# Performance work log

Hardware: AMD Instinct MI355X
Metric: run time of the kernel (lower is better)

Reference implementation:

```python
import jax, jax.numpy as jnp
import numpy as np

N, DM, F, G, FG = 4096, 512, 128, 8, 16
DH, DE, ES = 128, 256, 4
E = G * ES
GROUP_TOP_K, EXPERT_TOP_K = 2, 2
TEMP = 1.0
LN_EPS = 1e-5


def _ln(x, g, b):
    m = jnp.mean(x, axis=-1, keepdims=True)
    v = jnp.mean((x - m) ** 2, axis=-1, keepdims=True)
    return (x - m) * jax.lax.rsqrt(v + LN_EPS) * g + b


def _topk_softmax(logits, k):
    # faithful to torch _topk_softmax: softmax over top-k values, zeros elsewhere
    vals, idx = jax.lax.top_k(logits, k)
    w = jax.nn.softmax(vals, axis=-1)
    oh = jax.nn.one_hot(idx, logits.shape[-1], dtype=logits.dtype)  # [..., k, E]
    return jnp.einsum('...ke,...k->...e', oh, w)


def setup_inputs() -> dict:
    key = jax.random.key(0)
    ks = iter(jax.random.split(key, 32))
    n = lambda shape, s=0.02: jax.random.normal(next(ks), shape, dtype=jnp.float32) * s
    d = {
        'hidden': jax.random.normal(next(ks), (N, DM), dtype=jnp.float32),
        'feat': jax.random.normal(next(ks), (N, F), dtype=jnp.float32),
        # pre_ln
        'pre_ln_g': jnp.ones((DM,), jnp.float32), 'pre_ln_b': jnp.zeros((DM,), jnp.float32),
        # router_hidden_encoder: LN(DM) -> Lin(DM,DH) -> GELU -> Lin(DH,DH)
        'rh_ln_g': jnp.ones((DM,), jnp.float32), 'rh_ln_b': jnp.zeros((DM,), jnp.float32),
        'rh_w1': n((DM, DH)), 'rh_b1': jnp.zeros((DH,), jnp.float32),
        'rh_w2': n((DH, DH)), 'rh_b2': jnp.zeros((DH,), jnp.float32),
        # stage_feature_encoder: LN(F) -> Lin(F,DH) -> GELU -> Lin(DH,DH)
        'sf_ln_g': jnp.ones((F,), jnp.float32), 'sf_ln_b': jnp.zeros((F,), jnp.float32),
        'sf_w1': n((F, DH)), 'sf_b1': jnp.zeros((DH,), jnp.float32),
        'sf_w2': n((DH, DH)), 'sf_b2': jnp.zeros((DH,), jnp.float32),
        # group_feature_encoders (stacked over G): LN(FG) -> Lin(FG,DH) -> GELU -> Lin(DH,DH)
        'gf_ln_g': jnp.ones((G, FG), jnp.float32), 'gf_ln_b': jnp.zeros((G, FG), jnp.float32),
        'gf_w1': n((G, FG, DH)), 'gf_b1': jnp.zeros((G, DH), jnp.float32),
        'gf_w2': n((G, DH, DH)), 'gf_b2': jnp.zeros((G, DH), jnp.float32),
        # per_group_scorer (ScalarRouter): Lin(4DH,DH) -> GELU -> Lin(DH,1)
        'pgs_w1': n((4 * DH, DH)), 'pgs_b1': jnp.zeros((DH,), jnp.float32),
        'pgs_w2': n((DH,)), 'pgs_b2': jnp.zeros((), jnp.float32),
        # intra_routers (stacked over G): Lin(4DH,DH) -> GELU -> Lin(DH,ES)
        'ir_w1': n((G, 4 * DH, DH)), 'ir_b1': jnp.zeros((G, DH), jnp.float32),
        'ir_w2': n((G, DH, ES)), 'ir_b2': jnp.zeros((G, ES), jnp.float32),
        # experts (stacked over E = G*ES, group-major): Lin(DM,DE) -> GELU -> Lin(DE,DM)
        'ex_w1': n((E, DM, DE)), 'ex_b1': jnp.zeros((E, DE), jnp.float32),
        'ex_w2': n((E, DE, DM)), 'ex_b2': jnp.zeros((E, DM), jnp.float32),
    }
    return d


def reference(hidden, feat, pre_ln_g, pre_ln_b, rh_ln_g, rh_ln_b, rh_w1, rh_b1, rh_w2, rh_b2,
              sf_ln_g, sf_ln_b, sf_w1, sf_b1, sf_w2, sf_b2,
              gf_ln_g, gf_ln_b, gf_w1, gf_b1, gf_w2, gf_b2,
              pgs_w1, pgs_b1, pgs_w2, pgs_b2,
              ir_w1, ir_b1, ir_w2, ir_b2,
              ex_w1, ex_b1, ex_w2, ex_b2):
    # expert input (pre-LN hidden)
    h_norm = _ln(hidden, pre_ln_g, pre_ln_b)                         # [N, DM]

    # factorized router encoders
    h_enc = jax.nn.gelu(_ln(hidden, rh_ln_g, rh_ln_b) @ rh_w1 + rh_b1) @ rh_w2 + rh_b2   # [N, DH]
    s_enc = jax.nn.gelu(_ln(feat, sf_ln_g, sf_ln_b) @ sf_w1 + sf_b1) @ sf_w2 + sf_b2     # [N, DH]
    gfeat = feat.reshape(N, G, FG)                                    # disjoint contiguous group features
    g_h = jax.nn.gelu(jnp.einsum('ngf,gfh->ngh', _ln(gfeat, gf_ln_g, gf_ln_b), gf_w1) + gf_b1)
    g_enc = jnp.einsum('ngh,ghk->ngk', g_h, gf_w2) + gf_b2            # [N, G, DH]

    hB = jnp.broadcast_to(h_enc[:, None, :], (N, G, DH))
    sB = jnp.broadcast_to(s_enc[:, None, :], (N, G, DH))
    router_in = jnp.concatenate([hB, sB, g_enc, hB * g_enc], axis=-1)  # [N, G, 4DH]

    # per-group scalar scores -> group logits -> top-k scatter softmax
    pg_h = jax.nn.gelu(jnp.einsum('ngi,ih->ngh', router_in, pgs_w1) + pgs_b1)
    group_logits = (jnp.einsum('ngh,h->ng', pg_h, pgs_w2) + pgs_b2) / max(TEMP, 1e-6)    # [N, G]
    group_w = _topk_softmax(group_logits, GROUP_TOP_K)                 # [N, G]

    # intra-group expert routers -> top-k scatter softmax over expert_scale
    ir_h = jax.nn.gelu(jnp.einsum('ngi,gih->ngh', router_in, ir_w1) + ir_b1)
    intra_logits = jnp.einsum('ngh,ghe->nge', ir_h, ir_w2) + ir_b2     # [N, G, ES]
    intra_w = _topk_softmax(intra_logits, EXPERT_TOP_K)                # [N, G, ES]

    comb_w = (group_w[:, :, None] * intra_w).reshape(N, E)             # group-major expert order

    # per-expert GELU MLPs on pre-LN hidden (dense compute, sparse weights)
    eh = jax.nn.gelu(jnp.einsum('nd,edh->neh', h_norm, ex_w1) + ex_b1) # [N, E, DE]
    eo = jnp.einsum('neh,ehd->ned', eh, ex_w2) + ex_b2                 # [N, E, DM]
    out = jnp.einsum('ne,ned->nd', comb_w, eo)                         # [N, DM]
    return out
```

## Files before the change

### kernel.cpp

```cpp
#include <hip/hip_runtime.h>
#include <hip/hip_bf16.h>
#include <math.h>

#define N_TOK 4096
#define DM 512
#define FDIM 128
#define G 8
#define FG 16
#define DH 128
#define DE 256
#define ES 4
#define E_EXP 32
#define LN_EPS 1e-5f
#define BT 32

typedef __attribute__((ext_vector_type(8))) short bf16x8;
typedef __attribute__((ext_vector_type(4))) float f32x4;

#define MFMA16(a, b, c) __builtin_amdgcn_mfma_f32_16x16x32_bf16((a), (b), (c), 0, 0, 0)

#define PSTRIDE 6144

__device__ __forceinline__ float gelu_t(float x) {
    const float c = 0.7978845608028654f;
    float x3 = x * x * x;
    return 0.5f * x * (1.0f + tanhf(c * (x + 0.044715f * x3)));
}

__device__ __forceinline__ short f2bf(float f) {
    __hip_bfloat16 h = __float2bfloat16(f);
    return *reinterpret_cast<short*>(&h);
}
__device__ __forceinline__ float bf2f(short s) {
    __hip_bfloat16 h = *reinterpret_cast<__hip_bfloat16*>(&s);
    return __bfloat162float(h);
}
__device__ __forceinline__ void split3(float x, short& h, short& m, short& l) {
    h = f2bf(x);
    float r = x - bf2f(h);
    m = f2bf(r);
    float r2 = r - bf2f(m);
    l = f2bf(r2);
}

__device__ __forceinline__ void gload_lds16(const void* g, void* l) {
    __builtin_amdgcn_global_load_lds(
        (const __attribute__((address_space(1))) unsigned int*)g,
        (__attribute__((address_space(3))) unsigned int*)l, 16, 0, 0);
}

struct ConvJob { const float* src; short* dh; short* dm; short* dl;
                 int KB, NB, Kreal, plain, blk0; };
struct ConvJobs { ConvJob j[10]; };

__global__ void k_pre(ConvJobs J, int nconv,
                      const float* __restrict__ hidden,
                      const float* __restrict__ pg, const float* __restrict__ pb,
                      const float* __restrict__ rg, const float* __restrict__ rb,
                      __hip_bfloat16* __restrict__ h_normb, float* __restrict__ hL) {
    int b = blockIdx.x;
    if (b >= nconv) {
        int n = b - nconv;
        int j = threadIdx.x;
        const float* x = hidden + (size_t)n * DM;
        float v0 = x[j], v1 = x[j + 256];
        float s = v0 + v1, q = v0 * v0 + v1 * v1;
#pragma unroll
        for (int o = 32; o; o >>= 1) { s += __shfl_down(s, o); q += __shfl_down(q, o); }
        __shared__ float red[8];
        int w = j >> 6;
        if ((j & 63) == 0) { red[w] = s; red[4 + w] = q; }
        __syncthreads();
        float sum = red[0] + red[1] + red[2] + red[3];
        float sq  = red[4] + red[5] + red[6] + red[7];
        float m = sum * (1.0f / DM);
        float var = sq * (1.0f / DM) - m * m;
        float rs = rsqrtf(var + LN_EPS);
        float t0 = (v0 - m) * rs, t1 = (v1 - m) * rs;
        size_t base = (size_t)n * DM;
        h_normb[base + j]       = __float2bfloat16(t0 * pg[j]       + pb[j]);
        h_normb[base + j + 256] = __float2bfloat16(t1 * pg[j + 256] + pb[j + 256]);
        hL[base + j]           = t0 * rg[j]       + rb[j];
        hL[base + j + 256]     = t1 * rg[j + 256] + rb[j + 256];
        return;
    }
    int ji = 0;
#pragma unroll
    for (int i = 1; i < 10; i++) if (b >= J.j[i].blk0) ji = i;
    const ConvJob jb = J.j[ji];
    int rel = b - jb.blk0;
    int mat = rel / jb.KB, kb = rel % jb.KB;
    int ncols = jb.NB * 16;
    const float* s = jb.src + (size_t)mat * jb.Kreal * ncols;
    size_t dbase = ((size_t)mat * jb.KB + kb) * jb.NB * 512;
    for (int p = threadIdx.x; p < jb.NB * 64; p += 256) {
        int nb = p >> 6, lane = p & 63;
        int row0 = kb * 32 + ((lane >> 4) << 3);
        int col = nb * 16 + (lane & 15);
        if (jb.plain) {
            union { short sh[8]; uint4 v; } t;
#pragma unroll
            for (int j = 0; j < 8; j++) {
                float x = (row0 + j < jb.Kreal) ? s[(size_t)(row0 + j) * ncols + col] : 0.f;
                t.sh[j] = f2bf(x);
            }
            *(uint4*)&jb.dh[dbase + (size_t)p * 8] = t.v;
        } else {
            union { short sh[8]; uint4 v; } hi, mi, lo;
#pragma unroll
            for (int j = 0; j < 8; j++) {
                float x = (row0 + j < jb.Kreal) ? s[(size_t)(row0 + j) * ncols + col] : 0.f;
                split3(x, hi.sh[j], mi.sh[j], lo.sh[j]);
            }
            *(uint4*)&jb.dh[dbase + (size_t)p * 8] = hi.v;
            *(uint4*)&jb.dm[dbase + (size_t)p * 8] = mi.v;
            *(uint4*)&jb.dl[dbase + (size_t)p * 8] = lo.v;
        }
    }
}

__device__ __forceinline__ void emit_split_tiles(
        int tid, short (*Ah)[136], short (*Am)[136], short (*Al)[136],
        short* __restrict__ Yt, size_t panel0 ) {
    int lane_ = tid & 63, w = tid >> 6;
#pragma unroll
    for (int j = 0; j < 6; j++) {
        int combo = w * 6 + j;
        int split = combo >> 3;
        int rem = combo & 7; int t16 = rem >> 2, kb = rem & 3;
        const short* sp = (split == 0) ? &Ah[0][0] : (split == 1) ? &Am[0][0] : &Al[0][0];
        uint4 v = *(const uint4*)&sp[(t16 * 16 + (lane_ & 15)) * 136 + kb * 32 + (lane_ >> 4) * 8];
        *(uint4*)&Yt[((panel0 + t16) * 4 + kb) * 1536 + split * 512 + lane_ * 8] = v;
    }
}

template <int KB_TOT, bool DO_LN>
__device__ __forceinline__ void enc2_body(
        int bx, char* smem,
        const float* __restrict__ X,
        const float* __restrict__ lng, const float* __restrict__ lnb,
        const short* __restrict__ W1h, const short* __restrict__ W1m, const short* __restrict__ W1l,
        const float* __restrict__ B1,
        const short* __restrict__ W2h, const short* __restrict__ W2m, const short* __restrict__ W2l,
        const float* __restrict__ B2,
        short* __restrict__ Yt) {
    constexpr int K = KB_TOT * 32;
    const int n0 = bx * 32;
    const int tid = threadIdx.x;
    const int wave = tid >> 6, lane = tid & 63;
    const int quad = lane >> 4, lm = lane & 15;
    const int mt = wave & 1;
    const int ngb = (wave >> 1) * 4;

    short (*Ah)[136] = (short(*)[136])smem;
    short (*Am)[136] = (short(*)[136])(smem + 8704);
    short (*Al)[136] = (short(*)[136])(smem + 2 * 8704);

    f32x4 acc[4];
#pragma unroll
    for (int i = 0; i < 4; i++) acc[i] = (f32x4)(0.f);

    if (DO_LN) {
        for (int idx = tid; idx < 1024; idx += 256) {
            int row = idx >> 5, c4 = (idx & 31) * 4;
            float4 v = *(const float4*)&X[(size_t)(n0 + row) * K + c4];
            float s = v.x + v.y + v.z + v.w;
            float q = v.x * v.x + v.y * v.y + v.z * v.z + v.w * v.w;
#pragma unroll
            for (int o = 16; o; o >>= 1) { s += __shfl_xor(s, o); q += __shfl_xor(q, o); }
            float mean = s * (1.0f / 128.0f);
            float var = q * (1.0f / 128.0f) - mean * mean;
            float rs = rsqrtf(var + LN_EPS);
            float xv[4] = {(v.x - mean) * rs * lng[c4 + 0] + lnb[c4 + 0],
                           (v.y - mean) * rs * lng[c4 + 1] + lnb[c4 + 1],
                           (v.z - mean) * rs * lng[c4 + 2] + lnb[c4 + 2],
                           (v.w - mean) * rs * lng[c4 + 3] + lnb[c4 + 3]};
#pragma unroll
            for (int j = 0; j < 4; j++) {
                short h, m, l; split3(xv[j], h, m, l);
                Ah[row][c4 + j] = h; Am[row][c4 + j] = m; Al[row][c4 + j] = l;
            }
        }
        __syncthreads();
#pragma unroll
        for (int kb = 0; kb < KB_TOT; kb++) {
            bf16x8 ah = *(const bf16x8*)&Ah[mt * 16 + lm][kb * 32 + quad * 8];
            bf16x8 am = *(const bf16x8*)&Am[mt * 16 + lm][kb * 32 + quad * 8];
            bf16x8 al = *(const bf16x8*)&Al[mt * 16 + lm][kb * 32 + quad * 8];
#pragma unroll
            for (int nt = 0; nt < 4; nt++) {
                size_t bi = (((size_t)kb * 8 + ngb + nt) * 64 + lane) * 8;
                bf16x8 bh = *(const bf16x8*)&W1h[bi];
                bf16x8 bm = *(const bf16x8*)&W1m[bi];
                bf16x8 bl = *(const bf16x8*)&W1l[bi];
                acc[nt] = MFMA16(al, bh, acc[nt]);
                acc[nt] = MFMA16(am, bm, acc[nt]);
                acc[nt] = MFMA16(ah, bl, acc[nt]);
                acc[nt] = MFMA16(am, bh, acc[nt]);
                acc[nt] = MFMA16(ah, bm, acc[nt]);
                acc[nt] = MFMA16(ah, bh, acc[nt]);
            }
        }
    } else {
        for (int kb = 0; kb < KB_TOT; kb++) {
            const float* xs = X + (size_t)(n0 + mt * 16 + lm) * K + kb * 32 + quad * 8;
            float4 x0 = *(const float4*)xs, x1 = *(const float4*)(xs + 4);
            float xv[8] = {x0.x, x0.y, x0.z, x0.w, x1.x, x1.y, x1.z, x1.w};
            bf16x8 ah, am, al;
#pragma unroll
            for (int j = 0; j < 8; j++) {
                short h, m, l; split3(xv[j], h, m, l);
                ah[j] = h; am[j] = m; al[j] = l;
            }
#pragma unroll
            for (int nt = 0; nt < 4; nt++) {
                size_t bi = (((size_t)kb * 8 + ngb + nt) * 64 + lane) * 8;
                bf16x8 bh = *(const bf16x8*)&W1h[bi];
                bf16x8 bm = *(const bf16x8*)&W1m[bi];
                bf16x8 bl = *(const bf16x8*)&W1l[bi];
                acc[nt] = MFMA16(al, bh, acc[nt]);
                acc[nt] = MFMA16(am, bm, acc[nt]);
                acc[nt] = MFMA16(ah, bl, acc[nt]);
                acc[nt] = MFMA16(am, bh, acc[nt]);
                acc[nt] = MFMA16(ah, bm, acc[nt]);
                acc[nt] = MFMA16(ah, bh, acc[nt]);
            }
        }
    }
    __syncthreads();
#pragma unroll
    for (int nt = 0; nt < 4; nt++) {
        int col = (ngb + nt) * 16 + lm;
        float b1 = B1[col];
#pragma unroll
        for (int r = 0; r < 4; r++) {
            int row = mt * 16 + quad * 4 + r;
            short h, m, l; split3(gelu_t(acc[nt][r] + b1), h, m, l);
            Ah[row][col] = h; Am[row][col] = m; Al[row][col] = l;
        }
    }
    __syncthreads();
    f32x4 acc2[4];
#pragma unroll
    for (int i = 0; i < 4; i++) acc2[i] = (f32x4)(0.f);
#pragma unroll
    for (int kb = 0; kb < 4; kb++) {
        bf16x8 ah = *(const bf16x8*)&Ah[mt * 16 + lm][kb * 32 + quad * 8];
        bf16x8 am = *(const bf16x8*)&Am[mt * 16 + lm][kb * 32 + quad * 8];
        bf16x8 al = *(const bf16x8*)&Al[mt * 16 + lm][kb * 32 + quad * 8];
#pragma unroll
        for (int nt = 0; nt < 4; nt++) {
            size_t bi = (((size_t)kb * 8 + ngb + nt) * 64 + lane) * 8;
            bf16x8 bh = *(const bf16x8*)&W2h[bi];
            bf16x8 bm = *(const bf16x8*)&W2m[bi];
            bf16x8 bl = *(const bf16x8*)&W2l[bi];
            acc2[nt] = MFMA16(al, bh, acc2[nt]);
            acc2[nt] = MFMA16(am, bm, acc2[nt]);
            acc2[nt] = MFMA16(ah, bl, acc2[nt]);
            acc2[nt] = MFMA16(am, bh, acc2[nt]);
            acc2[nt] = MFMA16(ah, bm, acc2[nt]);
            acc2[nt] = MFMA16(ah, bh, acc2[nt]);
        }
    }
    __syncthreads();
#pragma unroll
    for (int nt = 0; nt < 4; nt++) {
        int col = (ngb + nt) * 16 + lm;
        float b2 = B2[col];
#pragma unroll
        for (int r = 0; r < 4; r++) {
            int row = mt * 16 + quad * 4 + r;
            short h, m, l; split3(acc2[nt][r] + b2, h, m, l);
            Ah[row][col] = h; Am[row][col] = m; Al[row][col] = l;
        }
    }
    __syncthreads();
    emit_split_tiles(tid, Ah, Am, Al, Yt, (size_t)bx * 2);
}

__device__ __forceinline__ void genc_one(
        int bx, int g, char* smem,
        const float* __restrict__ feat,
        const float* __restrict__ gln_g, const float* __restrict__ gln_b,
        const short* __restrict__ W1h, const short* __restrict__ W1m, const short* __restrict__ W1l,
        const float* __restrict__ gb1,
        const short* __restrict__ W2h, const short* __restrict__ W2m, const short* __restrict__ W2l,
        const float* __restrict__ gb2,
        short* __restrict__ Gs) {
    const int tid = threadIdx.x;
    const int wave = tid >> 6, lane = tid & 63;
    const int quad = lane >> 4, lm = lane & 15;
    const int mt = wave & 1;
    const int ngb = (wave >> 1) * 4;
    const int n0 = bx * 32;

    short (*Ah)[136] = (short(*)[136])smem;
    short (*Am)[136] = (short(*)[136])(smem + 8704);
    short (*Al)[136] = (short(*)[136])(smem + 2 * 8704);

    {
        int t = tid >> 3, sub = tid & 7;
        const float* fr = feat + (size_t)(n0 + t) * FDIM + g * FG;
        float xv[FG];
        float mean = 0.f;
#pragma unroll
        for (int i = 0; i < FG; i++) { xv[i] = fr[i]; mean += xv[i]; }
        mean *= (1.0f / FG);
        float var = 0.f;
#pragma unroll
        for (int i = 0; i < FG; i++) { float d = xv[i] - mean; var += d * d; }
        var *= (1.0f / FG);
        float rs = rsqrtf(var + LN_EPS);
#pragma unroll
        for (int j = 0; j < 2; j++) {
            int i = sub * 2 + j;
            float xn = (xv[i] - mean) * rs * gln_g[g * FG + i] + gln_b[g * FG + i];
            short h, m, l; split3(xn, h, m, l);
            Ah[t][i] = h; Am[t][i] = m; Al[t][i] = l;
            Ah[t][16 + i] = 0; Am[t][16 + i] = 0; Al[t][16 + i] = 0;
        }
    }
    __syncthreads();
    f32x4 acc[4];
#pragma unroll
    for (int i = 0; i < 4; i++) acc[i] = (f32x4)(0.f);
    {
        bf16x8 ah = *(const bf16x8*)&Ah[mt * 16 + lm][quad * 8];
        bf16x8 am = *(const bf16x8*)&Am[mt * 16 + lm][quad * 8];
        bf16x8 al = *(const bf16x8*)&Al[mt * 16 + lm][quad * 8];
#pragma unroll
        for (int nt = 0; nt < 4; nt++) {
            size_t bi = (((size_t)g * 8 + ngb + nt) * 64 + lane) * 8;
            bf16x8 bh = *(const bf16x8*)&W1h[bi];
            bf16x8 bm = *(const bf16x8*)&W1m[bi];
            bf16x8 bl = *(const bf16x8*)&W1l[bi];
            acc[nt] = MFMA16(al, bh, acc[nt]);
            acc[nt] = MFMA16(am, bm, acc[nt]);
            acc[nt] = MFMA16(ah, bl, acc[nt]);
            acc[nt] = MFMA16(am, bh, acc[nt]);
            acc[nt] = MFMA16(ah, bm, acc[nt]);
            acc[nt] = MFMA16(ah, bh, acc[nt]);
        }
    }
    __syncthreads();
#pragma unroll
    for (int nt = 0; nt < 4; nt++) {
        int col = (ngb + nt) * 16 + lm;
        float b1 = gb1[g * DH + col];
#pragma unroll
        for (int r = 0; r < 4; r++) {
            int row = mt * 16 + quad * 4 + r;
            short h, m, l; split3(gelu_t(acc[nt][r] + b1), h, m, l);
            Ah[row][col] = h; Am[row][col] = m; Al[row][col] = l;
        }
    }
    __syncthreads();
    f32x4 acc2[4];
#pragma unroll
    for (int i = 0; i < 4; i++) acc2[i] = (f32x4)(0.f);
#pragma unroll
    for (int kb = 0; kb < 4; kb++) {
        bf16x8 a2h = *(const bf16x8*)&Ah[mt * 16 + lm][kb * 32 + quad * 8];
        bf16x8 a2m = *(const bf16x8*)&Am[mt * 16 + lm][kb * 32 + quad * 8];
        bf16x8 a2l = *(const bf16x8*)&Al[mt * 16 + lm][kb * 32 + quad * 8];
#pragma unroll
        for (int nt = 0; nt < 4; nt++) {
            size_t bi = ((((size_t)g * 4 + kb) * 8 + ngb + nt) * 64 + lane) * 8;
            bf16x8 bh = *(const bf16x8*)&W2h[bi];
            bf16x8 bm = *(const bf16x8*)&W2m[bi];
            bf16x8 bl = *(const bf16x8*)&W2l[bi];
            acc2[nt] = MFMA16(a2l, bh, acc2[nt]);
            acc2[nt] = MFMA16(a2m, bm, acc2[nt]);
            acc2[nt] = MFMA16(a2h, bl, acc2[nt]);
            acc2[nt] = MFMA16(a2m, bh, acc2[nt]);
            acc2[nt] = MFMA16(a2h, bm, acc2[nt]);
            acc2[nt] = MFMA16(a2h, bh, acc2[nt]);
        }
    }
    __syncthreads();
#pragma unroll
    for (int nt = 0; nt < 4; nt++) {
        int col = (ngb + nt) * 16 + lm;
        float b2 = gb2[g * DH + col];
#pragma unroll
        for (int r = 0; r < 4; r++) {
            int row = mt * 16 + quad * 4 + r;
            short h, m, l; split3(acc2[nt][r] + b2, h, m, l);
            Ah[row][col] = h; Am[row][col] = m; Al[row][col] = l;
        }
    }
    __syncthreads();
    emit_split_tiles(tid, Ah, Am, Al, Gs, (size_t)g * 256 + bx * 2);
}

__global__ __launch_bounds__(256) void k_enc_all(
        const float* __restrict__ hL, const float* __restrict__ feat,
        const float* __restrict__ sf_g, const float* __restrict__ sf_b,
        const float* __restrict__ gln_g, const float* __restrict__ gln_b,
        const short* Brh1H, const short* Brh1M, const short* Brh1L, const float* rh_b1,
        const short* Brh2H, const short* Brh2M, const short* Brh2L, const float* rh_b2,
        const short* Bsf1H, const short* Bsf1M, const short* Bsf1L, const float* sf_b1,
        const short* Bsf2H, const short* Bsf2M, const short* Bsf2L, const float* sf_b2,
        const short* Bgf1H, const short* Bgf1M, const short* Bgf1L, const float* gf_b1,
        const short* Bgf2H, const short* Bgf2M, const short* Bgf2L, const float* gf_b2,
        short* __restrict__ Hs, short* __restrict__ Ss, short* __restrict__ Gs) {
    __shared__ __align__(16) char smem[3 * 8704];
    int bid = blockIdx.x;
    if (bid < 128)
        enc2_body<16, false>(bid, smem, hL, nullptr, nullptr,
                             Brh1H, Brh1M, Brh1L, rh_b1, Brh2H, Brh2M, Brh2L, rh_b2, Hs);
    else if (bid < 256)
        enc2_body<4, true>(bid - 128, smem, feat, sf_g, sf_b,
                           Bsf1H, Bsf1M, Bsf1L, sf_b1, Bsf2H, Bsf2M, Bsf2L, sf_b2, Ss);
    else {
        int idx = bid - 256;
        genc_one(idx >> 3, idx & 7, smem, feat, gln_g, gln_b,
                 Bgf1H, Bgf1M, Bgf1L, gf_b1, Bgf2H, Bgf2M, Bgf2L, gf_b2, Gs);
    }
}

__global__ __launch_bounds__(512) void k_router_mfma(
        const short* __restrict__ Hs, const short* __restrict__ Ss, const short* __restrict__ Gs,
        const short* __restrict__ BpgH, const short* __restrict__ BpgM, const short* __restrict__ BpgL,
        const short* __restrict__ BirH, const short* __restrict__ BirM, const short* __restrict__ BirL,
        const float* __restrict__ pb1, const float* __restrict__ pw2, const float* __restrict__ pb2,
        const float* __restrict__ ib1, const float* __restrict__ iw2, const float* __restrict__ ib2,
        float* __restrict__ glog, float* __restrict__ ilog) {
    const int g = blockIdx.x & 7;
    const int bx = blockIdx.x >> 3;
    const int n0 = bx * 64;
    const int tid = threadIdx.x;
    const int wave = tid >> 6, lane = tid & 63;
    const int quad = lane >> 4, lm = lane & 15;
    const bool is_pg = wave < 4;
    const int nbase = (wave & 3) * 2;
    const short* Bh = is_pg ? BpgH : (BirH + (size_t)g * 65536);
    const short* Bm = is_pg ? BpgM : (BirM + (size_t)g * 65536);
    const short* Bl = is_pg ? BpgL : (BirL + (size_t)g * 65536);

    const short* HsB = Hs + (size_t)bx * 4 * PSTRIDE;
    const short* SsB = Ss + (size_t)bx * 4 * PSTRIDE;
    const short* GsB = Gs + ((size_t)g * 256 + bx * 4) * PSTRIDE;

    __shared__ __align__(16) char smem[49152];

    f32x4 acc[4][2];
#pragma unroll
    for (int mt = 0; mt < 4; mt++)
#pragma unroll
        for (int nt = 0; nt < 2; nt++) acc[mt][nt] = (f32x4)(0.f);

    for (int ch = 0; ch < 4; ch++) {
        __syncthreads();
        if (ch < 3) {
            const short* base = (ch == 0) ? HsB : (ch == 1) ? SsB : GsB;
#pragma unroll
            for (int it = 0; it < 6; it++) {
                int combo = wave * 6 + it;
                int split = combo >> 4;
                int rem = combo & 15; int kbl = rem >> 2, t16 = rem & 3;
                const short* gp = base + (size_t)t16 * PSTRIDE + kbl * 1536 + split * 512 + lane * 8;
                char* lp = smem + split * 16384 + kbl * 4096 + t16 * 1024;
                gload_lds16(gp, lp);
            }
        } else {
            for (int idx = tid; idx < 1024; idx += 512) {
                int kbl = idx >> 8, rem = idx & 255;
                int t16 = rem >> 6, lane2 = rem & 63;
                size_t loff = (size_t)kbl * 4096 + t16 * 1024 + (size_t)lane2 * 16;
                bf16x8 gh = *(const bf16x8*)(smem + loff);
                bf16x8 gm = *(const bf16x8*)(smem + 16384 + loff);
                bf16x8 gl = *(const bf16x8*)(smem + 32768 + loff);
                const short* hp = HsB + (size_t)t16 * PSTRIDE + kbl * 1536 + lane2 * 8;
                bf16x8 hh8 = *(const bf16x8*)hp;
                bf16x8 hm8 = *(const bf16x8*)(hp + 512);
                bf16x8 hl8 = *(const bf16x8*)(hp + 1024);
                union { short sh[8]; uint4 v; } oh, om, ol;
#pragma unroll
                for (int j = 0; j < 8; j++) {
                    float gv = bf2f(gh[j]) + bf2f(gm[j]) + bf2f(gl[j]);
                    float hv = bf2f(hh8[j]) + bf2f(hm8[j]) + bf2f(hl8[j]);
                    short a_, b_, c_; split3(hv * gv, a_, b_, c_);
                    oh.sh[j] = a_; om.sh[j] = b_; ol.sh[j] = c_;
                }
                *(uint4*)(smem + loff) = oh.v;
                *(uint4*)(smem + 16384 + loff) = om.v;
                *(uint4*)(smem + 32768 + loff) = ol.v;
            }
        }
        __syncthreads();
#pragma unroll
        for (int kbl = 0; kbl < 4; kbl++) {
            int kb = ch * 4 + kbl;
            bf16x8 Ahf[4], Amf[4], Alf[4];
#pragma unroll
            for (int mt = 0; mt < 4; mt++) {
                size_t loff = (size_t)kbl * 4096 + mt * 1024 + (size_t)lane * 16;
                Ahf[mt] = *(const bf16x8*)(smem + loff);
                Amf[mt] = *(const bf16x8*)(smem + 16384 + loff);
                Alf[mt] = *(const bf16x8*)(smem + 32768 + loff);
            }
#pragma unroll
            for (int nt = 0; nt < 2; nt++) {
                int nb = nbase + nt;
                size_t bi = (((size_t)kb * 8 + nb) * 64 + lane) * 8;
                bf16x8 bh = *(const bf16x8*)&Bh[bi];
                bf16x8 bm = *(const bf16x8*)&Bm[bi];
                bf16x8 bl = *(const bf16x8*)&Bl[bi];
#pragma unroll
                for (int mt = 0; mt < 4; mt++) {
                    acc[mt][nt] = MFMA16(Alf[mt], bh, acc[mt][nt]);
                    acc[mt][nt] = MFMA16(Amf[mt], bm, acc[mt][nt]);
                    acc[mt][nt] = MFMA16(Ahf[mt], bl, acc[mt][nt]);
                    acc[mt][nt] = MFMA16(Amf[mt], bh, acc[mt][nt]);
                    acc[mt][nt] = MFMA16(Ahf[mt], bm, acc[mt][nt]);
                    acc[mt][nt] = MFMA16(Ahf[mt], bh, acc[mt][nt]);
                }
            }
        }
    }

    float (*ph)[129] = (float(*)[129])smem;
    float (*ih)[129] = (float(*)[129])(smem + 32 * 129 * 4);
    for (int h = 0; h < 2; h++) {
        __syncthreads();
#pragma unroll
        for (int mi = 0; mi < 2; mi++) {
            int mt = 2 * h + mi;
#pragma unroll
            for (int nt = 0; nt < 2; nt++) {
                int col = (nbase + nt) * 16 + lm;
                float b1 = is_pg ? pb1[col] : ib1[g * DH + col];
                float* dst = is_pg ? &ph[0][0] : &ih[0][0];
#pragma unroll
                for (int r = 0; r < 4; r++) {
                    int row = mi * 16 + quad * 4 + r;
                    dst[row * 129 + col] = gelu_t(acc[mt][nt][r] + b1);
                }
            }
        }
        __syncthreads();
        if (tid < 128) {
            int t = tid >> 2, q = tid & 3;
            float s = 0.f;
            for (int i = q * 32; i < q * 32 + 32; i++) s += ph[t][i] * pw2[i];
            s += __shfl_xor(s, 1);
            s += __shfl_xor(s, 2);
            if (q == 0) glog[(size_t)(n0 + h * 32 + t) * G + g] = s + pb2[0];
        } else if (tid < 384) {
            int t2 = tid - 128;
            int t = t2 >> 3, e = (t2 >> 1) & 3, half = t2 & 1;
            const float* wv = iw2 + (size_t)g * DH * ES;
            float s = 0.f;
            for (int i = half * 64; i < half * 64 + 64; i++) s += ih[t][i] * wv[i * ES + e];
            s += __shfl_xor(s, 1);
            if (half == 0) ilog[((size_t)(n0 + h * 32 + t) * G + g) * ES + e] = s + ib2[g * ES + e];
        }
    }
}

__global__ void k_topk(const float* __restrict__ glog, const float* __restrict__ ilog,
                       int* __restrict__ cnt, int* __restrict__ toks, float* __restrict__ wgts) {
    int n = blockIdx.x * blockDim.x + threadIdx.x;
    if (n >= N_TOK) return;
    float gl[G];
#pragma unroll
    for (int g = 0; g < G; g++) gl[g] = glog[(size_t)n * G + g];
    int i1 = 0; float v1 = gl[0];
#pragma unroll
    for (int g = 1; g < G; g++) if (gl[g] > v1) { v1 = gl[g]; i1 = g; }
    int i2 = -1; float v2 = -1e30f;
#pragma unroll
    for (int g = 0; g < G; g++) if (g != i1 && gl[g] > v2) { v2 = gl[g]; i2 = g; }
    float eg = expf(v2 - v1);
    float den = 1.0f / (1.0f + eg);
    float gw_sel[2] = { den, eg * den };
    int g_sel[2] = { i1, i2 };
#pragma unroll
    for (int s = 0; s < 2; s++) {
        int g = g_sel[s]; float gw = gw_sel[s];
        float il[ES];
#pragma unroll
        for (int e = 0; e < ES; e++) il[e] = ilog[((size_t)n * G + g) * ES + e];
        int j1 = 0; float u1 = il[0];
#pragma unroll
        for (int e = 1; e < ES; e++) if (il[e] > u1) { u1 = il[e]; j1 = e; }
        int j2 = -1; float u2 = -1e30f;
#pragma unroll
        for (int e = 0; e < ES; e++) if (e != j1 && il[e] > u2) { u2 = il[e]; j2 = e; }
        float ei = expf(u2 - u1);
        float d2 = 1.0f / (1.0f + ei);
        int ex1 = g * ES + j1, ex2 = g * ES + j2;
        int p1 = atomicAdd(&cnt[ex1], 1);
        toks[(size_t)ex1 * N_TOK + p1] = n * 4 + s * 2;     wgts[(size_t)ex1 * N_TOK + p1] = gw * d2;
        int p2 = atomicAdd(&cnt[ex2], 1);
        toks[(size_t)ex2 * N_TOK + p2] = n * 4 + s * 2 + 1; wgts[(size_t)ex2 * N_TOK + p2] = gw * ei * d2;
    }
}

__global__ __launch_bounds__(512) void k_expert_mfma(
        const __hip_bfloat16* __restrict__ h_normb,
        const short* __restrict__ wB1, const float* __restrict__ eb1,
        const short* __restrict__ wB2, const float* __restrict__ eb2,
        const int* __restrict__ cnt, const int* __restrict__ toks,
        const float* __restrict__ wgts, float* __restrict__ part) {
    const int e = blockIdx.x & 31;
    const int slot = blockIdx.x >> 5;
    const int c = cnt[e];
    const int start = slot * BT;
    if (start >= c) return;
    const int m = min(BT, c - start);

    __shared__ short hs[BT][520];
    short (*es)[264] = (short(*)[264])&hs[0][0];
    __shared__ int   tok_s[BT];
    __shared__ float w_s[BT];

    const int tid = threadIdx.x;
    if (tid < BT) {
        bool ok = tid < m;
        tok_s[tid] = ok ? toks[(size_t)e * N_TOK + start + tid] : 0;
        w_s[tid]   = ok ? wgts[(size_t)e * N_TOK + start + tid] : 0.f;
    }
    __syncthreads();
    for (int idx = tid; idx < BT * 64; idx += 512) {
        int t = idx >> 6, ch = idx & 63;
        uint4 v = make_uint4(0, 0, 0, 0);
        if (t < m) v = *((const uint4*)(h_normb + (size_t)(tok_s[t] >> 2) * DM) + ch);
        *(uint4*)&hs[t][ch * 8] = v;
    }
    __syncthreads();

    const int wave = tid >> 6, lane = tid & 63;
    const int quad = lane >> 4, lm = lane & 15;

    const int ng = wave * 2;
    f32x4 acc1[2][2];
#pragma unroll
    for (int a = 0; a < 2; a++)
#pragma unroll
        for (int b = 0; b < 2; b++) acc1[a][b] = (f32x4)(0.f);
    {
        const short* w1e = wB1 + (size_t)e * DM * DE;
        for (int kb = 0; kb < 16; kb++) {
            bf16x8 a0 = *(const bf16x8*)&hs[lm][kb * 32 + quad * 8];
            bf16x8 a1 = *(const bf16x8*)&hs[16 + lm][kb * 32 + quad * 8];
            const short* wp = w1e + ((size_t)kb * 16 + ng) * 512 + lane * 8;
#pragma unroll
            for (int nt = 0; nt < 2; nt++) {
                bf16x8 b = *(const bf16x8*)(wp + nt * 512);
                acc1[0][nt] = MFMA16(a0, b, acc1[0][nt]);
                acc1[1][nt] = MFMA16(a1, b, acc1[1][nt]);
            }
        }
    }
    __syncthreads();
#pragma unroll
    for (int nt = 0; nt < 2; nt++) {
        int col = (ng + nt) * 16 + lm;
        float b1 = eb1[e * DE + col];
#pragma unroll
        for (int mt = 0; mt < 2; mt++)
#pragma unroll
        for (int r = 0; r < 4; r++) {
            int row = mt * 16 + quad * 4 + r;
            es[row][col] = f2bf(gelu_t(acc1[mt][nt][r] + b1));
        }
    }
    __syncthreads();

    {
        const int ng2 = wave * 4;
        f32x4 acc[2][4];
#pragma unroll
        for (int a = 0; a < 2; a++)
#pragma unroll
            for (int b = 0; b < 4; b++) acc[a][b] = (f32x4)(0.f);
        const short* w2e = wB2 + (size_t)e * DE * DM;
        for (int kb = 0; kb < 8; kb++) {
            bf16x8 a0 = *(const bf16x8*)&es[lm][kb * 32 + quad * 8];
            bf16x8 a1 = *(const bf16x8*)&es[16 + lm][kb * 32 + quad * 8];
            const short* wp = w2e + ((size_t)kb * 32 + ng2) * 512 + lane * 8;
#pragma unroll
            for (int nt = 0; nt < 4; nt++) {
                bf16x8 b = *(const bf16x8*)(wp + nt * 512);
                acc[0][nt] = MFMA16(a0, b, acc[0][nt]);
                acc[1][nt] = MFMA16(a1, b, acc[1][nt]);
            }
        }
        const float* b2 = eb2 + (size_t)e * DM;
#pragma unroll
        for (int mt = 0; mt < 2; mt++)
#pragma unroll
        for (int r = 0; r < 4; r++) {
            int row = mt * 16 + quad * 4 + r;
            if (row < m) {
                float w = w_s[row];
                float* prow = part + (size_t)tok_s[row] * DM;
#pragma unroll
                for (int nt = 0; nt < 4; nt++) {
                    int col = (ng2 + nt) * 16 + lm;
                    prow[col] = w * (acc[mt][nt][r] + b2[col]);
                }
            }
        }
    }
}

__global__ void k_reduce(const float* __restrict__ part, float* __restrict__ out) {
    int n = blockIdx.x;
    int j = threadIdx.x;
    const float4* p = (const float4*)(part + (size_t)n * 4 * DM);
    float4 a = p[j], b = p[128 + j], c = p[256 + j], d = p[384 + j];
    float4 r = make_float4(a.x + b.x + c.x + d.x, a.y + b.y + c.y + d.y,
                           a.z + b.z + c.z + d.z, a.w + b.w + c.w + d.w);
    ((float4*)(out + (size_t)n * DM))[j] = r;
}

extern "C" void kernel_launch(void* const* d_in, const int* in_sizes, int n_in,
                              void* d_out, int out_size, void* d_ws, size_t ws_size,
                              hipStream_t stream) {
    const float* hidden  = (const float*)d_in[0];
    const float* feat    = (const float*)d_in[1];
    const float* pre_g   = (const float*)d_in[2];
    const float* pre_b   = (const float*)d_in[3];
    const float* rh_g    = (const float*)d_in[4];
    const float* rh_b    = (const float*)d_in[5];
    const float* rh_w1   = (const float*)d_in[6];
    const float* rh_b1   = (const float*)d_in[7];
    const float* rh_w2   = (const float*)d_in[8];
    const float* rh_b2   = (const float*)d_in[9];
    const float* sf_g    = (const float*)d_in[10];
    const float* sf_b    = (const float*)d_in[11];
    const float* sf_w1   = (const float*)d_in[12];
    const float* sf_b1   = (const float*)d_in[13];
    const float* sf_w2   = (const float*)d_in[14];
    const float* sf_b2   = (const float*)d_in[15];
    const float* gln_g   = (const float*)d_in[16];
    const float* gln_b   = (const float*)d_in[17];
    const float* gf_w1   = (const float*)d_in[18];
    const float* gf_b1   = (const float*)d_in[19];
    const float* gf_w2   = (const float*)d_in[20];
    const float* gf_b2   = (const float*)d_in[21];
    const float* pgs_w1  = (const float*)d_in[22];
    const float* pgs_b1  = (const float*)d_in[23];
    const float* pgs_w2  = (const float*)d_in[24];
    const float* pgs_b2  = (const float*)d_in[25];
    const float* ir_w1   = (const float*)d_in[26];
    const float* ir_b1   = (const float*)d_in[27];
    const float* ir_w2   = (const float*)d_in[28];
    const float* ir_b2   = (const float*)d_in[29];
    const float* ex_w1   = (const float*)d_in[30];
    const float* ex_b1   = (const float*)d_in[31];
    const float* ex_w2   = (const float*)d_in[32];
    const float* ex_b2   = (const float*)d_in[33];
    float* out = (float*)d_out;

    char* w = (char*)d_ws;
    auto alloc = [&](size_t bytes) { void* r = (void*)w; w += (bytes + 255) & ~(size_t)255; return r; };
    __hip_bfloat16* h_normb = (__hip_bfloat16*)alloc((size_t)N_TOK * DM * 2);
    short* Hs    = (short*)alloc((size_t)256 * PSTRIDE * 2);
    short* Ss    = (short*)alloc((size_t)256 * PSTRIDE * 2);
    float* glog  = (float*)alloc((size_t)N_TOK * G * 4);
    float* ilog  = (float*)alloc((size_t)N_TOK * G * ES * 4);
    float* wgts  = (float*)alloc((size_t)E_EXP * N_TOK * 4);
    short* wB1   = (short*)alloc((size_t)E_EXP * DM * DE * 2);
    short* wB2   = (short*)alloc((size_t)E_EXP * DE * DM * 2);
    short* BpgH  = (short*)alloc((size_t)16 * 8 * 512 * 2);
    short* BpgM  = (short*)alloc((size_t)16 * 8 * 512 * 2);
    short* BpgL  = (short*)alloc((size_t)16 * 8 * 512 * 2);
    short* BirH  = (short*)alloc((size_t)G * 16 * 8 * 512 * 2);
    short* BirM  = (short*)alloc((size_t)G * 16 * 8 * 512 * 2);
    short* BirL  = (short*)alloc((size_t)G * 16 * 8 * 512 * 2);
    short* Brh1H = (short*)alloc((size_t)16 * 8 * 512 * 2);
    short* Brh1M = (short*)alloc((size_t)16 * 8 * 512 * 2);
    short* Brh1L = (short*)alloc((size_t)16 * 8 * 512 * 2);
    short* Brh2H = (short*)alloc((size_t)4 * 8 * 512 * 2);
    short* Brh2M = (short*)alloc((size_t)4 * 8 * 512 * 2);
    short* Brh2L = (short*)alloc((size_t)4 * 8 * 512 * 2);
    short* Bsf1H = (short*)alloc((size_t)4 * 8 * 512 * 2);
    short* Bsf1M = (short*)alloc((size_t)4 * 8 * 512 * 2);
    short* Bsf1L = (short*)alloc((size_t)4 * 8 * 512 * 2);
    short* Bsf2H = (short*)alloc((size_t)4 * 8 * 512 * 2);
    short* Bsf2M = (short*)alloc((size_t)4 * 8 * 512 * 2);
    short* Bsf2L = (short*)alloc((size_t)4 * 8 * 512 * 2);
    short* Bgf1H = (short*)alloc((size_t)G * 1 * 8 * 512 * 2);
    short* Bgf1M = (short*)alloc((size_t)G * 1 * 8 * 512 * 2);
    short* Bgf1L = (short*)alloc((size_t)G * 1 * 8 * 512 * 2);
    short* Bgf2H = (short*)alloc((size_t)G * 4 * 8 * 512 * 2);
    short* Bgf2M = (short*)alloc((size_t)G * 4 * 8 * 512 * 2);
    short* Bgf2L = (short*)alloc((size_t)G * 4 * 8 * 512 * 2);
    int* cnt     = (int*)alloc(E_EXP * 4);
    int* toks    = (int*)alloc((size_t)E_EXP * N_TOK * 4);
    char* uni   = (char*)alloc((size_t)N_TOK * 4 * DM * 4);
    float* hL   = (float*)uni;
    short* Gs   = (short*)(uni + (size_t)N_TOK * DM * 4);
    float* part = (float*)uni;

    hipMemsetAsync(cnt, 0, E_EXP * sizeof(int), stream);

    ConvJobs J;
    int b0 = 0;
    auto mkjob = [&](int i, const float* s, short* dh, short* dm, short* dl,
                     int KB, int NB, int Kreal, int plain, int nmat) {
        J.j[i] = ConvJob{s, dh, dm, dl, KB, NB, Kreal, plain, b0};
        b0 += KB * nmat;
    };
    mkjob(0, ex_w1, wB1, nullptr, nullptr, 16, 16, 512, 1, E_EXP);
    mkjob(1, ex_w2, wB2, nullptr, nullptr, 8, 32, 256, 1, E_EXP);
    mkjob(2, pgs_w1, BpgH, BpgM, BpgL, 16, 8, 512, 0, 1);
    mkjob(3, ir_w1, BirH, BirM, BirL, 16, 8, 512, 0, G);
    mkjob(4, rh_w1, Brh1H, Brh1M, Brh1L, 16, 8, 512, 0, 1);
    mkjob(5, rh_w2, Brh2H, Brh2M, Brh2L, 4, 8, 128, 0, 1);
    mkjob(6, sf_w1, Bsf1H, Bsf1M, Bsf1L, 4, 8, 128, 0, 1);
    mkjob(7, sf_w2, Bsf2H, Bsf2M, Bsf2L, 4, 8, 128, 0, 1);
    mkjob(8, gf_w1, Bgf1H, Bgf1M, Bgf1L, 1, 8, 16, 0, G);
    mkjob(9, gf_w2, Bgf2H, Bgf2M, Bgf2L, 4, 8, 128, 0, G);
    k_pre<<<b0 + N_TOK, 256, 0, stream>>>(J, b0, hidden, pre_g, pre_b, rh_g, rh_b, h_normb, hL);

    k_enc_all<<<256 + (N_TOK / 32) * G, 256, 0, stream>>>(
        hL, feat, sf_g, sf_b, gln_g, gln_b,
        Brh1H, Brh1M, Brh1L, rh_b1, Brh2H, Brh2M, Brh2L, rh_b2,
        Bsf1H, Bsf1M, Bsf1L, sf_b1, Bsf2H, Bsf2M, Bsf2L, sf_b2,
        Bgf1H, Bgf1M, Bgf1L, gf_b1, Bgf2H, Bgf2M, Bgf2L, gf_b2,
        Hs, Ss, Gs);

    k_router_mfma<<<(N_TOK / 64) * G, 512, 0, stream>>>(Hs, Ss, Gs,
                                             BpgH, BpgM, BpgL, BirH, BirM, BirL,
                                             pgs_b1, pgs_w2, pgs_b2, ir_b1, ir_w2, ir_b2,
                                             glog, ilog);

    k_topk<<<N_TOK / 256, 256, 0, stream>>>(glog, ilog, cnt, toks, wgts);
    k_expert_mfma<<<(N_TOK / BT) * E_EXP, 512, 0, stream>>>(h_normb, wB1, ex_b1, wB2, ex_b2,
                                                            cnt, toks, wgts, part);
    k_reduce<<<N_TOK, 128, 0, stream>>>(part, out);
}
```

Measured before the change: 339.0 us.

## Software-pipeline router operand loads through registers to overlap with MFMA

Replaces the direct global-to-LDS loads in the router kernel with register-staged prefetching. The next chunk's operands are loaded into registers while MFMAs run on the current chunk. The hB*g_enc product chunk is computed from globally loaded H and G values during chunk 2's compute, instead of a separate LDS read-modify-write phase. It also adds a min-blocks-per-CU launch bound, which increases register pressure from the prefetch buffers and risks spills.

```diff
diff --git a/kernel.cpp b/kernel.cpp
--- a/kernel.cpp
+++ b/kernel.cpp
@@ -41,12 +41,6 @@
     m = f2bf(r);
     float r2 = r - bf2f(m);
     l = f2bf(r2);
-}
-
-__device__ __forceinline__ void gload_lds16(const void* g, void* l) {
-    __builtin_amdgcn_global_load_lds(
-        (const __attribute__((address_space(1))) unsigned int*)g,
-        (__attribute__((address_space(3))) unsigned int*)l, 16, 0, 0);
 }
 
 struct ConvJob { const float* src; short* dh; short* dm; short* dl;
@@ -419,7 +413,7 @@
     }
 }
 
-__global__ __launch_bounds__(512) void k_router_mfma(
+__global__ __launch_bounds__(512, 4) void k_router_mfma(
         const short* __restrict__ Hs, const short* __restrict__ Ss, const short* __restrict__ Gs,
         const short* __restrict__ BpgH, const short* __restrict__ BpgM, const short* __restrict__ BpgL,
         const short* __restrict__ BirH, const short* __restrict__ BirM, const short* __restrict__ BirL,
@@ -444,51 +438,62 @@
 
     __shared__ __align__(16) char smem[49152];
 
+    int goff[6];
+#pragma unroll
+    for (int it = 0; it < 6; it++) {
+        int lin = it * 512 + tid;
+        int split = lin >> 10, rem = lin & 1023;
+        int kbl = rem >> 8, t16 = (rem >> 6) & 3, ln = rem & 63;
+        goff[it] = t16 * PSTRIDE + kbl * 1536 + split * 512 + ln * 8;
+    }
+    int roff[2], woff[2];
+#pragma unroll
+    for (int t = 0; t < 2; t++) {
+        int slot = t * 512 + tid;
+        int kbl = slot >> 8, t16 = (slot >> 6) & 3, ln = slot & 63;
+        roff[t] = t16 * PSTRIDE + kbl * 1536 + ln * 8;
+        woff[t] = kbl * 4096 + t16 * 1024 + ln * 16;
+    }
+
     f32x4 acc[4][2];
 #pragma unroll
     for (int mt = 0; mt < 4; mt++)
 #pragma unroll
         for (int nt = 0; nt < 2; nt++) acc[mt][nt] = (f32x4)(0.f);
+
+    bf16x8 R[6];
+    bf16x8 R3[2][3];
+#pragma unroll
+    for (int it = 0; it < 6; it++) R[it] = *(const bf16x8*)(HsB + goff[it]);
 
     for (int ch = 0; ch < 4; ch++) {
         __syncthreads();
         if (ch < 3) {
-            const short* base = (ch == 0) ? HsB : (ch == 1) ? SsB : GsB;
-#pragma unroll
-            for (int it = 0; it < 6; it++) {
-                int combo = wave * 6 + it;
-                int split = combo >> 4;
-                int rem = combo & 15; int kbl = rem >> 2, t16 = rem & 3;
-                const short* gp = base + (size_t)t16 * PSTRIDE + kbl * 1536 + split * 512 + lane * 8;
-                char* lp = smem + split * 16384 + kbl * 4096 + t16 * 1024;
-                gload_lds16(gp, lp);
-            }
+#pragma unroll
+            for (int it = 0; it < 6; it++)
+                *(bf16x8*)(smem + ((it * 512 + tid) * 16)) = R[it];
         } else {
-            for (int idx = tid; idx < 1024; idx += 512) {
-                int kbl = idx >> 8, rem = idx & 255;
-                int t16 = rem >> 6, lane2 = rem & 63;
-                size_t loff = (size_t)kbl * 4096 + t16 * 1024 + (size_t)lane2 * 16;
-                bf16x8 gh = *(const bf16x8*)(smem + loff);
-                bf16x8 gm = *(const bf16x8*)(smem + 16384 + loff);
-                bf16x8 gl = *(const bf16x8*)(smem + 32768 + loff);
-                const short* hp = HsB + (size_t)t16 * PSTRIDE + kbl * 1536 + lane2 * 8;
-                bf16x8 hh8 = *(const bf16x8*)hp;
-                bf16x8 hm8 = *(const bf16x8*)(hp + 512);
-                bf16x8 hl8 = *(const bf16x8*)(hp + 1024);
-                union { short sh[8]; uint4 v; } oh, om, ol;
-#pragma unroll
-                for (int j = 0; j < 8; j++) {
-                    float gv = bf2f(gh[j]) + bf2f(gm[j]) + bf2f(gl[j]);
-                    float hv = bf2f(hh8[j]) + bf2f(hm8[j]) + bf2f(hl8[j]);
-                    short a_, b_, c_; split3(hv * gv, a_, b_, c_);
-                    oh.sh[j] = a_; om.sh[j] = b_; ol.sh[j] = c_;
+#pragma unroll
+            for (int t = 0; t < 2; t++)
+#pragma unroll
+                for (int s = 0; s < 3; s++)
+                    *(bf16x8*)(smem + s * 16384 + woff[t]) = R3[t][s];
+        }
+        __syncthreads();
+        bf16x8 Hv[2][3], Gv[2][3];
+        if (ch < 2) {
+            const short* nb = (ch == 0) ? SsB : GsB;
+#pragma unroll
+            for (int it = 0; it < 6; it++) R[it] = *(const bf16x8*)(nb + goff[it]);
+        } else if (ch == 2) {
+#pragma unroll
+            for (int t = 0; t < 2; t++)
+#pragma unroll
+                for (int s = 0; s < 3; s++) {
+                    Hv[t][s] = *(const bf16x8*)(HsB + roff[t] + s * 512);
+                    Gv[t][s] = *(const bf16x8*)(GsB + roff[t] + s * 512);
                 }
-                *(uint4*)(smem + loff) = oh.v;
-                *(uint4*)(smem + 16384 + loff) = om.v;
-                *(uint4*)(smem + 32768 + loff) = ol.v;
-            }
-        }
-        __syncthreads();
+        }
 #pragma unroll
         for (int kbl = 0; kbl < 4; kbl++) {
             int kb = ch * 4 + kbl;
@@ -516,6 +521,20 @@
                     acc[mt][nt] = MFMA16(Ahf[mt], bm, acc[mt][nt]);
                     acc[mt][nt] = MFMA16(Ahf[mt], bh, acc[mt][nt]);
                 }
+            }
+        }
+        if (ch == 2) {
+#pragma unroll
+            for (int t = 0; t < 2; t++) {
+                bf16x8 oa, ob, oc;
+#pragma unroll
+                for (int j = 0; j < 8; j++) {
+                    float hv = bf2f(Hv[t][0][j]) + bf2f(Hv[t][1][j]) + bf2f(Hv[t][2][j]);
+                    float gv = bf2f(Gv[t][0][j]) + bf2f(Gv[t][1][j]) + bf2f(Gv[t][2][j]);
+                    short a_, b_, c_; split3(hv * gv, a_, b_, c_);
+                    oa[j] = a_; ob[j] = b_; oc[j] = c_;
+                }
+                R3[t][0] = oa; R3[t][1] = ob; R3[t][2] = oc;
             }
         }
     }
```

Measured after the change: 457.7 us. +35.0%, slower.

## Register-prefetch next router-input chunk while computing current chunk

Applied to the files above, without the earlier changes.

Replaces the direct global-to-LDS loads with register-staged prefetch, so each chunk's global loads are issued before the MFMA compute of the previous chunk and then written to LDS. The h*g product chunk is also computed from global loads issued ahead, instead of a separate LDS read-modify-write pass. This is meant to hide global load latency behind MFMA work in the router scoring kernel, at the cost of more VGPRs for the staged registers and possibly lower occupancy.

```diff
diff --git a/kernel.cpp b/kernel.cpp
--- a/kernel.cpp
+++ b/kernel.cpp
@@ -41,12 +41,6 @@
     m = f2bf(r);
     float r2 = r - bf2f(m);
     l = f2bf(r2);
-}
-
-__device__ __forceinline__ void gload_lds16(const void* g, void* l) {
-    __builtin_amdgcn_global_load_lds(
-        (const __attribute__((address_space(1))) unsigned int*)g,
-        (__attribute__((address_space(3))) unsigned int*)l, 16, 0, 0);
 }
 
 struct ConvJob { const float* src; short* dh; short* dm; short* dl;
@@ -444,81 +438,125 @@
 
     __shared__ __align__(16) char smem[49152];
 
+    int goff[6];
+#pragma unroll
+    for (int it = 0; it < 6; it++) {
+        int lin = it * 512 + tid;
+        int split = lin >> 10, rem = lin & 1023;
+        int kbl = rem >> 8, t16 = (rem >> 6) & 3, ln = rem & 63;
+        goff[it] = t16 * PSTRIDE + kbl * 1536 + split * 512 + ln * 8;
+    }
+    int roff0, roff1, woff0, woff1;
+    {
+        int slot = tid;
+        int kbl = slot >> 8, t16 = (slot >> 6) & 3, ln = slot & 63;
+        roff0 = t16 * PSTRIDE + kbl * 1536 + ln * 8;
+        woff0 = kbl * 4096 + t16 * 1024 + ln * 16;
+        slot = 512 + tid;
+        kbl = slot >> 8; t16 = (slot >> 6) & 3; ln = slot & 63;
+        roff1 = t16 * PSTRIDE + kbl * 1536 + ln * 8;
+        woff1 = kbl * 4096 + t16 * 1024 + ln * 16;
+    }
+
     f32x4 acc[4][2];
 #pragma unroll
     for (int mt = 0; mt < 4; mt++)
 #pragma unroll
         for (int nt = 0; nt < 2; nt++) acc[mt][nt] = (f32x4)(0.f);
 
-    for (int ch = 0; ch < 4; ch++) {
-        __syncthreads();
-        if (ch < 3) {
-            const short* base = (ch == 0) ? HsB : (ch == 1) ? SsB : GsB;
-#pragma unroll
-            for (int it = 0; it < 6; it++) {
-                int combo = wave * 6 + it;
-                int split = combo >> 4;
-                int rem = combo & 15; int kbl = rem >> 2, t16 = rem & 3;
-                const short* gp = base + (size_t)t16 * PSTRIDE + kbl * 1536 + split * 512 + lane * 8;
-                char* lp = smem + split * 16384 + kbl * 4096 + t16 * 1024;
-                gload_lds16(gp, lp);
-            }
-        } else {
-            for (int idx = tid; idx < 1024; idx += 512) {
-                int kbl = idx >> 8, rem = idx & 255;
-                int t16 = rem >> 6, lane2 = rem & 63;
-                size_t loff = (size_t)kbl * 4096 + t16 * 1024 + (size_t)lane2 * 16;
-                bf16x8 gh = *(const bf16x8*)(smem + loff);
-                bf16x8 gm = *(const bf16x8*)(smem + 16384 + loff);
-                bf16x8 gl = *(const bf16x8*)(smem + 32768 + loff);
-                const short* hp = HsB + (size_t)t16 * PSTRIDE + kbl * 1536 + lane2 * 8;
-                bf16x8 hh8 = *(const bf16x8*)hp;
-                bf16x8 hm8 = *(const bf16x8*)(hp + 512);
-                bf16x8 hl8 = *(const bf16x8*)(hp + 1024);
-                union { short sh[8]; uint4 v; } oh, om, ol;
-#pragma unroll
-                for (int j = 0; j < 8; j++) {
-                    float gv = bf2f(gh[j]) + bf2f(gm[j]) + bf2f(gl[j]);
-                    float hv = bf2f(hh8[j]) + bf2f(hm8[j]) + bf2f(hl8[j]);
-                    short a_, b_, c_; split3(hv * gv, a_, b_, c_);
-                    oh.sh[j] = a_; om.sh[j] = b_; ol.sh[j] = c_;
-                }
-                *(uint4*)(smem + loff) = oh.v;
-                *(uint4*)(smem + 16384 + loff) = om.v;
-                *(uint4*)(smem + 32768 + loff) = ol.v;
-            }
-        }
-        __syncthreads();
-#pragma unroll
-        for (int kbl = 0; kbl < 4; kbl++) {
-            int kb = ch * 4 + kbl;
-            bf16x8 Ahf[4], Amf[4], Alf[4];
-#pragma unroll
-            for (int mt = 0; mt < 4; mt++) {
-                size_t loff = (size_t)kbl * 4096 + mt * 1024 + (size_t)lane * 16;
-                Ahf[mt] = *(const bf16x8*)(smem + loff);
-                Amf[mt] = *(const bf16x8*)(smem + 16384 + loff);
-                Alf[mt] = *(const bf16x8*)(smem + 32768 + loff);
-            }
-#pragma unroll
-            for (int nt = 0; nt < 2; nt++) {
-                int nb = nbase + nt;
-                size_t bi = (((size_t)kb * 8 + nb) * 64 + lane) * 8;
-                bf16x8 bh = *(const bf16x8*)&Bh[bi];
-                bf16x8 bm = *(const bf16x8*)&Bm[bi];
-                bf16x8 bl = *(const bf16x8*)&Bl[bi];
-#pragma unroll
-                for (int mt = 0; mt < 4; mt++) {
-                    acc[mt][nt] = MFMA16(Alf[mt], bh, acc[mt][nt]);
-                    acc[mt][nt] = MFMA16(Amf[mt], bm, acc[mt][nt]);
-                    acc[mt][nt] = MFMA16(Ahf[mt], bl, acc[mt][nt]);
-                    acc[mt][nt] = MFMA16(Amf[mt], bh, acc[mt][nt]);
-                    acc[mt][nt] = MFMA16(Ahf[mt], bm, acc[mt][nt]);
-                    acc[mt][nt] = MFMA16(Ahf[mt], bh, acc[mt][nt]);
-                }
-            }
-        }
-    }
+    bf16x8 R[6];
+
+#define LOADR(basep) { _Pragma("unroll") \
+    for (int it = 0; it < 6; it++) R[it] = *(const bf16x8*)((basep) + goff[it]); }
+#define STAGE_WRITE() { _Pragma("unroll") \
+    for (int it = 0; it < 6; it++) *(bf16x8*)(smem + ((it * 512 + tid) * 16)) = R[it]; }
+#define COMPUTE_CHUNK(CH) { _Pragma("unroll") \
+    for (int kbl = 0; kbl < 4; kbl++) { \
+        const int kb = (CH) * 4 + kbl; \
+        bf16x8 Ahf[4], Amf[4], Alf[4]; \
+        _Pragma("unroll") \
+        for (int mt = 0; mt < 4; mt++) { \
+            size_t loff = (size_t)kbl * 4096 + mt * 1024 + (size_t)lane * 16; \
+            Ahf[mt] = *(const bf16x8*)(smem + loff); \
+            Amf[mt] = *(const bf16x8*)(smem + 16384 + loff); \
+            Alf[mt] = *(const bf16x8*)(smem + 32768 + loff); \
+        } \
+        _Pragma("unroll") \
+        for (int nt = 0; nt < 2; nt++) { \
+            size_t bi = (((size_t)kb * 8 + nbase + nt) * 64 + lane) * 8; \
+            bf16x8 bh = *(const bf16x8*)&Bh[bi]; \
+            bf16x8 bm = *(const bf16x8*)&Bm[bi]; \
+            bf16x8 bl = *(const bf16x8*)&Bl[bi]; \
+            _Pragma("unroll") \
+            for (int mt = 0; mt < 4; mt++) { \
+                acc[mt][nt] = MFMA16(Alf[mt], bh, acc[mt][nt]); \
+                acc[mt][nt] = MFMA16(Amf[mt], bm, acc[mt][nt]); \
+                acc[mt][nt] = MFMA16(Ahf[mt], bl, acc[mt][nt]); \
+                acc[mt][nt] = MFMA16(Amf[mt], bh, acc[mt][nt]); \
+                acc[mt][nt] = MFMA16(Ahf[mt], bm, acc[mt][nt]); \
+                acc[mt][nt] = MFMA16(Ahf[mt], bh, acc[mt][nt]); \
+            } \
+        } \
+    } }
+
+    LOADR(HsB);
+    STAGE_WRITE();
+    __syncthreads();
+    LOADR(SsB);
+    COMPUTE_CHUNK(0);
+
+    __syncthreads();
+    STAGE_WRITE();
+    __syncthreads();
+    LOADR(GsB);
+    COMPUTE_CHUNK(1);
+
+    __syncthreads();
+    STAGE_WRITE();
+    __syncthreads();
+    bf16x8 Hv0_0 = *(const bf16x8*)(HsB + roff0);
+    bf16x8 Hv0_1 = *(const bf16x8*)(HsB + roff0 + 512);
+    bf16x8 Hv0_2 = *(const bf16x8*)(HsB + roff0 + 1024);
+    bf16x8 Gv0_0 = *(const bf16x8*)(GsB + roff0);
+    bf16x8 Gv0_1 = *(const bf16x8*)(GsB + roff0 + 512);
+    bf16x8 Gv0_2 = *(const bf16x8*)(GsB + roff0 + 1024);
+    bf16x8 Hv1_0 = *(const bf16x8*)(HsB + roff1);
+    bf16x8 Hv1_1 = *(const bf16x8*)(HsB + roff1 + 512);
+    bf16x8 Hv1_2 = *(const bf16x8*)(HsB + roff1 + 1024);
+    bf16x8 Gv1_0 = *(const bf16x8*)(GsB + roff1);
+    bf16x8 Gv1_1 = *(const bf16x8*)(GsB + roff1 + 512);
+    bf16x8 Gv1_2 = *(const bf16x8*)(GsB + roff1 + 1024);
+    COMPUTE_CHUNK(2);
+
+    bf16x8 P0h, P0m, P0l, P1h, P1m, P1l;
+#pragma unroll
+    for (int j = 0; j < 8; j++) {
+        float hv = bf2f(Hv0_0[j]) + bf2f(Hv0_1[j]) + bf2f(Hv0_2[j]);
+        float gv = bf2f(Gv0_0[j]) + bf2f(Gv0_1[j]) + bf2f(Gv0_2[j]);
+        short a_, b_, c_; split3(hv * gv, a_, b_, c_);
+        P0h[j] = a_; P0m[j] = b_; P0l[j] = c_;
+    }
+#pragma unroll
+    for (int j = 0; j < 8; j++) {
+        float hv = bf2f(Hv1_0[j]) + bf2f(Hv1_1[j]) + bf2f(Hv1_2[j]);
+        float gv = bf2f(Gv1_0[j]) + bf2f(Gv1_1[j]) + bf2f(Gv1_2[j]);
+        short a_, b_, c_; split3(hv * gv, a_, b_, c_);
+        P1h[j] = a_; P1m[j] = b_; P1l[j] = c_;
+    }
+
+    __syncthreads();
+    *(bf16x8*)(smem + woff0)         = P0h;
+    *(bf16x8*)(smem + 16384 + woff0) = P0m;
+    *(bf16x8*)(smem + 32768 + woff0) = P0l;
+    *(bf16x8*)(smem + woff1)         = P1h;
+    *(bf16x8*)(smem + 16384 + woff1) = P1m;
+    *(bf16x8*)(smem + 32768 + woff1) = P1l;
+    __syncthreads();
+    COMPUTE_CHUNK(3);
+
+#undef LOADR
+#undef STAGE_WRITE
+#undef COMPUTE_CHUNK
 
     float (*ph)[129] = (float(*)[129])smem;
     float (*ih)[129] = (float(*)[129])(smem + 32 * 129 * 4);
```

Measured after the change: 345.6 us. About the same (+1.9%).
